# Kernel tuning notes

Measured on AMD Instinct MI355X. Metric: run time of the kernel, lower is better.

The kernel has to match this reference:

```python
import jax, jax.numpy as jnp
import numpy as np


def _lstm_layer(x, w_ih, w_hh, b_ih, b_hh):
    """Single PyTorch-style LSTM layer (gate order i,f,g,o). x: [B,T,D] -> [B,T,H]."""
    B, T, _ = x.shape
    H = w_hh.shape[1]
    # Precompute input projections for all timesteps (one big GEMM).
    xp = jnp.einsum('btd,gd->btg', x, w_ih) + b_ih + b_hh  # [B,T,4H]

    def step(carry, xt):
        h, c = carry
        gates = xt + h @ w_hh.T  # [B,4H]
        i, f, g, o = jnp.split(gates, 4, axis=-1)
        i = jax.nn.sigmoid(i)
        f = jax.nn.sigmoid(f)
        g = jnp.tanh(g)
        o = jax.nn.sigmoid(o)
        c = f * c + i * g
        h = o * jnp.tanh(c)
        return (h, c), h

    init = (jnp.zeros((B, H), x.dtype), jnp.zeros((B, H), x.dtype))
    _, hs = jax.lax.scan(step, init, jnp.swapaxes(xp, 0, 1))  # hs: [T,B,H]
    return jnp.swapaxes(hs, 0, 1)


def setup_inputs() -> dict:
    key = jax.random.key(0)
    ks = jax.random.split(key, 11)
    B, T, D, H, O = 256, 512, 64, 512, 1
    s_in = 1.0 / np.sqrt(H)
    inp = {
        'x': jax.random.normal(ks[0], (B, T, D), jnp.float32),
        'w_ih_0': jax.random.normal(ks[1], (4 * H, D), jnp.float32) * s_in,
        'w_hh_0': jax.random.normal(ks[2], (4 * H, H), jnp.float32) * s_in,
        'b_ih_0': jax.random.normal(ks[3], (4 * H,), jnp.float32) * s_in,
        'b_hh_0': jax.random.normal(ks[4], (4 * H,), jnp.float32) * s_in,
        'w_ih_1': jax.random.normal(ks[5], (4 * H, H), jnp.float32) * s_in,
        'w_hh_1': jax.random.normal(ks[6], (4 * H, H), jnp.float32) * s_in,
        'b_ih_1': jax.random.normal(ks[7], (4 * H,), jnp.float32) * s_in,
        'b_hh_1': jax.random.normal(ks[8], (4 * H,), jnp.float32) * s_in,
        'fc_w': jax.random.normal(ks[9], (O, H), jnp.float32) * s_in,
        'fc_b': jax.random.normal(ks[10], (O,), jnp.float32) * s_in,
    }
    return inp


def reference(x, w_ih_0, w_hh_0, b_ih_0, b_hh_0,
              w_ih_1, w_hh_1, b_ih_1, b_hh_1, fc_w, fc_b):
    h0 = _lstm_layer(x, w_ih_0, w_hh_0, b_ih_0, b_hh_0)   # [B,T,H]
    h1 = _lstm_layer(h0, w_ih_1, w_hh_1, b_ih_1, b_hh_1)  # [B,T,H]
    # fc on last timestep only
    return h1[:, -1, :] @ fc_w.T + fc_b  # [B,O]
```

## Files before the change

kernel.cpp:

```cpp
#include <hip/hip_runtime.h>


#define BATCH 256
#define SEQ   512
#define DIN   64
#define HID   512

typedef _Float16 f16_t;
typedef __attribute__((ext_vector_type(8))) _Float16 f16x8;
typedef __attribute__((ext_vector_type(4))) float    f32x4;

#define SCOPE_AGT __HIP_MEMORY_SCOPE_AGENT

__device__ inline f16x8 cvt8(const float* __restrict__ p) {
    f16x8 r;
#pragma unroll
    for (int j = 0; j < 8; j++) r[j] = (_Float16)p[j];
    return r;
}

__device__ inline f16x8 cvt8v(f32x4 lo, f32x4 hi) {
    f16x8 r;
#pragma unroll
    for (int j = 0; j < 4; j++) { r[j] = (_Float16)lo[j]; r[4 + j] = (_Float16)hi[j]; }
    return r;
}

__device__ inline f16x8 ldx8(const f16_t* p) {
    const unsigned long long* q = (const unsigned long long*)p;
    unsigned long long a = __hip_atomic_load(q,     __ATOMIC_RELAXED, SCOPE_AGT);
    unsigned long long b = __hip_atomic_load(q + 1, __ATOMIC_RELAXED, SCOPE_AGT);
    union { unsigned long long u[2]; f16x8 v; } c;
    c.u[0] = a; c.u[1] = b;
    return c.v;
}

__device__ inline void sth2a(f16_t* base_even, float h, float hn) {
    union { struct { _Float16 lo, hi; } s; unsigned u; } pk;
    pk.s.lo = (_Float16)h; pk.s.hi = (_Float16)hn;
    __hip_atomic_store((unsigned*)base_even, pk.u, __ATOMIC_RELAXED, SCOPE_AGT);
}

__device__ inline void pollw(const unsigned* p, unsigned need, int lane) {
    for (;;) {
        unsigned v = __hip_atomic_load(p + lane, __ATOMIC_RELAXED, SCOPE_AGT);
        if (__all((int)(v >= need))) break;
        __builtin_amdgcn_s_sleep(1);
    }
}

__device__ inline float sgm(float v) { return 1.f / (1.f + __expf(-v)); }
__device__ inline float th(float v)  { return 1.f - 2.f / (__expf(2.f * v) + 1.f); }

__global__ __launch_bounds__(256, 1) void lstm_pipe(
    const float* __restrict__ x,
    const float* __restrict__ wih0, const float* __restrict__ whh0,
    const float* __restrict__ bih0, const float* __restrict__ bhh0,
    const float* __restrict__ wih1, const float* __restrict__ whh1,
    const float* __restrict__ bih1, const float* __restrict__ bhh1,
    unsigned* __restrict__ f0m, unsigned* __restrict__ f1,
    f16_t* __restrict__ h1buf, f16_t* __restrict__ h0hist)
{
    __shared__ f32x4 red[5][17][64];

    const int tid  = threadIdx.x;
    const int w    = tid >> 6, lane = tid & 63;
    const int quad = lane >> 4, col = lane & 15;
    const int bid  = blockIdx.x;

    if (bid < 128) {
        const int g = bid & 7, s = bid >> 3;
        unsigned* myf = f0m + g * 64;
        const int mym = w & 1, myct = w >> 1;

        f16x8 Wh[32];
#pragma unroll
        for (int i = 0; i < 4; i++) {
            const int k0 = (w * 4 + i) * 32 + quad * 8;
#pragma unroll
            for (int ct = 0; ct < 2; ct++)
#pragma unroll
                for (int nt = 0; nt < 4; nt++) {
                    const int gr = nt * HID + s * 32 + ct * 16 + col;
                    Wh[i * 8 + ct * 4 + nt] = cvt8(whh0 + (size_t)gr * HID + k0);
                }
        }
        f16x8 Wx[8];
        if (w >= 2) {
#pragma unroll
            for (int ct = 0; ct < 2; ct++)
#pragma unroll
                for (int nt = 0; nt < 4; nt++) {
                    const int gr = nt * HID + s * 32 + ct * 16 + col;
                    Wx[ct * 4 + nt] = cvt8(wih0 + (size_t)gr * DIN + (w - 2) * 32 + quad * 8);
                }
        } else {
#pragma unroll
            for (int j = 0; j < 8; j++) Wx[j] = (f16x8)(_Float16)0;
        }
#pragma unroll
        for (int i = 0; i < 32; i++) asm volatile("" : "+v"(Wh[i]));
#pragma unroll
        for (int i = 0; i < 8; i++)  asm volatile("" : "+v"(Wx[i]));

        float bias[4];
#pragma unroll
        for (int nt = 0; nt < 4; nt++) {
            const int gr = nt * HID + s * 32 + myct * 16 + col;
            bias[nt] = bih0[gr] + bhh0[gr];
        }
        float cst[4] = {0, 0, 0, 0};

        for (int it = 0; it < SEQ; ++it) {
            {
                const f16_t* hw = h0hist + (size_t)it * BATCH * HID;
                unsigned sink = 0;
#pragma unroll
                for (int r = 0; r < 4; r++) {
                    const unsigned* p = (const unsigned*)(hw +
                        (size_t)(g * 32 + mym * 16 + quad * 4 + r) * HID + s * 32 + myct * 16 + (col & ~1));
                    sink += __hip_atomic_load(p, __ATOMIC_RELAXED, SCOPE_AGT);
                }
                asm volatile("" : "+v"(sink));
            }
            f32x4 xr[4];
            if (w >= 2) {
#pragma unroll
                for (int m = 0; m < 2; m++) {
                    const float* px = x + ((size_t)(g * 32 + m * 16 + col) * SEQ + it) * DIN + (w - 2) * 32 + quad * 8;
                    xr[m * 2]     = *(const f32x4*)px;
                    xr[m * 2 + 1] = *(const f32x4*)(px + 4);
                }
            }
            if (w == 0 && it >= 1) pollw(myf, (unsigned)it, lane);
            __syncthreads();

            f32x4 acc[16];
#pragma unroll
            for (int j = 0; j < 16; j++) acc[j] = (f32x4){0.f, 0.f, 0.f, 0.f};

            if (it > 0) {
                const f16_t* h0b = h0hist + (size_t)(it - 1) * BATCH * HID;
#pragma unroll
                for (int i = 0; i < 4; i++) {
                    const int kb = w * 4 + i;
#pragma unroll
                    for (int m = 0; m < 2; m++) {
                        f16x8 a = *(const f16x8*)(h0b + (size_t)(g * 32 + m * 16 + col) * HID + kb * 32 + quad * 8);
#pragma unroll
                        for (int ct = 0; ct < 2; ct++)
#pragma unroll
                            for (int nt = 0; nt < 4; nt++)
                                acc[m * 8 + ct * 4 + nt] = __builtin_amdgcn_mfma_f32_16x16x32_f16(
                                    a, Wh[i * 8 + ct * 4 + nt], acc[m * 8 + ct * 4 + nt], 0, 0, 0);
                    }
                }
            }
            if (w >= 2) {
#pragma unroll
                for (int m = 0; m < 2; m++) {
                    f16x8 a = cvt8v(xr[m * 2], xr[m * 2 + 1]);
#pragma unroll
                    for (int ct = 0; ct < 2; ct++)
#pragma unroll
                        for (int nt = 0; nt < 4; nt++)
                            acc[m * 8 + ct * 4 + nt] = __builtin_amdgcn_mfma_f32_16x16x32_f16(
                                a, Wx[ct * 4 + nt], acc[m * 8 + ct * 4 + nt], 0, 0, 0);
                }
            }
#pragma unroll
            for (int j = 0; j < 16; j++) red[w][j][lane] = acc[j];
            __syncthreads();

            f32x4 gate[4];
#pragma unroll
            for (int nt = 0; nt < 4; nt++) {
                f32x4 v = red[0][mym * 8 + myct * 4 + nt][lane];
#pragma unroll
                for (int ww = 1; ww < 4; ww++) {
                    f32x4 p = red[ww][mym * 8 + myct * 4 + nt][lane];
#pragma unroll
                    for (int r = 0; r < 4; r++) v[r] += p[r];
                }
                gate[nt] = v;
            }
            f16_t* hout = h0hist + (size_t)it * BATCH * HID;
#pragma unroll
            for (int r = 0; r < 4; r++) {
                float iv = sgm(gate[0][r] + bias[0]), fv = sgm(gate[1][r] + bias[1]);
                float gv = th(gate[2][r] + bias[2]),  ov = sgm(gate[3][r] + bias[3]);
                float c = fv * cst[r] + iv * gv;
                cst[r] = c;
                float h = ov * th(c);
                float hn = __shfl_down(h, 1);
                if ((lane & 1) == 0)
                    sth2a(hout + (size_t)(g * 32 + mym * 16 + quad * 4 + r) * HID + s * 32 + myct * 16 + col, h, hn);
            }
            asm volatile("s_waitcnt vmcnt(0)" ::: "memory");
            if (lane == 0)
                __hip_atomic_store(myf + s * 4 + mym * 2 + myct, (unsigned)(it + 1), __ATOMIC_RELAXED, SCOPE_AGT);
        }
    } else {
        const int idx = bid - 128;
        const int G = idx & 3, s1 = idx >> 2;
        unsigned* myf1 = f1 + G * 32;

        f16x8 Wb[32];
#pragma unroll
        for (int i = 0; i < 8; i++) {
            const int kb = w * 8 + i;
            const int k0 = kb * 32 + quad * 8;
#pragma unroll
            for (int nt = 0; nt < 4; nt++) {
                const int grow = nt * HID + s1 * 16 + col;
                const float* src = (kb < 16) ? (wih1 + (size_t)grow * HID + k0)
                                             : (whh1 + (size_t)grow * HID + (k0 - 512));
                Wb[i * 4 + nt] = cvt8(src);
            }
        }
#pragma unroll
        for (int i = 0; i < 32; i++) asm volatile("" : "+v"(Wb[i]));

        const int d = s1 * 16 + col;
        const float bi = bih1[d] + bhh1[d];
        const float bf = bih1[HID + d] + bhh1[HID + d];
        const float bg = bih1[2 * HID + d] + bhh1[2 * HID + d];
        const float bo = bih1[3 * HID + d] + bhh1[3 * HID + d];
        float cst[4] = {0, 0, 0, 0};

        for (int it = 1; it <= SEQ; ++it) {
            const int t = it - 1;
            if (w == 0) {
                const unsigned* pa = f0m + (2 * G) * 64;
                const unsigned* pb = f0m + (2 * G + 1) * 64;
                const bool chk = (it >= 2);
                for (;;) {
                    unsigned va = __hip_atomic_load(pa + lane, __ATOMIC_RELAXED, SCOPE_AGT);
                    unsigned vb = __hip_atomic_load(pb + lane, __ATOMIC_RELAXED, SCOPE_AGT);
                    unsigned vc = chk ? __hip_atomic_load(myf1 + (lane & 31), __ATOMIC_RELAXED, SCOPE_AGT)
                                      : 0xffffffffu;
                    if (__all((int)((va >= (unsigned)it) & (vb >= (unsigned)it) & (vc >= (unsigned)(it - 1))))) break;
                    __builtin_amdgcn_s_sleep(1);
                }
            }
            __syncthreads();

            f32x4 acc[16];
#pragma unroll
            for (int j = 0; j < 16; j++) acc[j] = (f32x4){0.f, 0.f, 0.f, 0.f};

            const f16_t* h0b = h0hist + (size_t)t * BATCH * HID;
            const f16_t* h1r = h1buf + (size_t)((t - 1) & 1) * BATCH * HID;
#pragma unroll
            for (int i = 0; i < 8; i++) {
                const int kb = w * 8 + i;
                if (kb < 16) {
#pragma unroll
                    for (int mt = 0; mt < 4; mt++) {
                        f16x8 a = *(const f16x8*)(h0b + (size_t)(G * 64 + mt * 16 + col) * HID + kb * 32 + quad * 8);
#pragma unroll
                        for (int nt = 0; nt < 4; nt++)
                            acc[mt * 4 + nt] = __builtin_amdgcn_mfma_f32_16x16x32_f16(
                                a, Wb[i * 4 + nt], acc[mt * 4 + nt], 0, 0, 0);
                    }
                } else if (t > 0) {
#pragma unroll
                    for (int mt = 0; mt < 4; mt++) {
                        f16x8 a = ldx8(h1r + (size_t)(G * 64 + mt * 16 + col) * HID + (kb - 16) * 32 + quad * 8);
#pragma unroll
                        for (int nt = 0; nt < 4; nt++)
                            acc[mt * 4 + nt] = __builtin_amdgcn_mfma_f32_16x16x32_f16(
                                a, Wb[i * 4 + nt], acc[mt * 4 + nt], 0, 0, 0);
                    }
                }
            }
#pragma unroll
            for (int j = 0; j < 16; j++) red[w][j][lane] = acc[j];
            __syncthreads();

            f32x4 gate[4];
#pragma unroll
            for (int nt = 0; nt < 4; nt++) {
                f32x4 v = red[0][w * 4 + nt][lane];
#pragma unroll
                for (int ww = 1; ww < 4; ww++) {
                    f32x4 p = red[ww][w * 4 + nt][lane];
#pragma unroll
                    for (int r = 0; r < 4; r++) v[r] += p[r];
                }
                gate[nt] = v;
            }
            f16_t* hout = h1buf + (size_t)(t & 1) * BATCH * HID;
#pragma unroll
            for (int r = 0; r < 4; r++) {
                float iv = sgm(gate[0][r] + bi), fv = sgm(gate[1][r] + bf);
                float gv = th(gate[2][r] + bg),  ov = sgm(gate[3][r] + bo);
                float c = fv * cst[r] + iv * gv;
                cst[r] = c;
                float h = ov * th(c);
                float hn = __shfl_down(h, 1);
                if ((lane & 1) == 0)
                    sth2a(hout + (size_t)(G * 64 + w * 16 + quad * 4 + r) * HID + s1 * 16 + col, h, hn);
            }
            __syncthreads();
            if (tid == 0)
                __hip_atomic_store(myf1 + s1, (unsigned)it, __ATOMIC_RELAXED, SCOPE_AGT);
        }
    }
}

__global__ void fc_k(const f16_t* __restrict__ h1buf, const float* __restrict__ fcw,
                     const float* __restrict__ fcb, float* __restrict__ out)
{
    const int b = blockIdx.x, lane = threadIdx.x;
    const f16_t* hp = h1buf + ((size_t)(BATCH + b)) * HID;
    float sum = 0.f;
#pragma unroll
    for (int j = 0; j < 8; j++) {
        const int k = lane * 8 + j;
        sum += (float)hp[k] * fcw[k];
    }
#pragma unroll
    for (int off = 32; off; off >>= 1) sum += __shfl_down(sum, off);
    if (lane == 0) out[b] = sum + fcb[0];
}

extern "C" void kernel_launch(void* const* d_in, const int* in_sizes, int n_in,
                              void* d_out, int out_size, void* d_ws, size_t ws_size,
                              hipStream_t stream)
{
    const float* x    = (const float*)d_in[0];
    const float* wih0 = (const float*)d_in[1];
    const float* whh0 = (const float*)d_in[2];
    const float* bih0 = (const float*)d_in[3];
    const float* bhh0 = (const float*)d_in[4];
    const float* wih1 = (const float*)d_in[5];
    const float* whh1 = (const float*)d_in[6];
    const float* bih1 = (const float*)d_in[7];
    const float* bhh1 = (const float*)d_in[8];
    const float* fcw  = (const float*)d_in[9];
    const float* fcb  = (const float*)d_in[10];
    float* out = (float*)d_out;

    unsigned char* ws = (unsigned char*)d_ws;
    unsigned* f0m = (unsigned*)ws;
    unsigned* f1  = (unsigned*)(ws + 2048);
    f16_t* h1buf  = (f16_t*)(ws + 4096);
    f16_t* h0hist = (f16_t*)(ws + 4096 + 2 * BATCH * HID * sizeof(f16_t));

    hipMemsetAsync(ws, 0, 4096, stream);
    lstm_pipe<<<dim3(256), dim3(256), 0, stream>>>(x, wih0, whh0, bih0, bhh0,
                                                   wih1, whh1, bih1, bhh1,
                                                   f0m, f1, h1buf, h0hist);
    fc_k<<<dim3(BATCH), dim3(64), 0, stream>>>(h1buf, fcw, fcb, out);
}
```

Measured before the change: 4.778 ms.

## Poll only needed producer flags per wave and drop a barrier via double-buffered reduction

Each wave now polls only the flags for the data it will read, so the step no longer waits on one poller wave followed by a block-wide barrier. The LDS reduction buffer is double-buffered by step parity so that removing the first __syncthreads does not let a fast wave overwrite partial sums still being read. In layer 1 the work is split into an h0 branch for waves 0-1 and an h1 branch for waves 2-3, each with its own wait condition. This shortens the per-step critical path across 512 sequential steps, but it puts more polling traffic on the flags and depends on the per-wave flag mapping being correct.

```diff
diff --git a/kernel.cpp b/kernel.cpp
--- a/kernel.cpp
+++ b/kernel.cpp
@@ -41,9 +41,9 @@
     __hip_atomic_store((unsigned*)base_even, pk.u, __ATOMIC_RELAXED, SCOPE_AGT);
 }
 
-__device__ inline void pollw(const unsigned* p, unsigned need, int lane) {
+__device__ inline void pollv(const unsigned* p, unsigned need) {
     for (;;) {
-        unsigned v = __hip_atomic_load(p + lane, __ATOMIC_RELAXED, SCOPE_AGT);
+        unsigned v = __hip_atomic_load(p, __ATOMIC_RELAXED, SCOPE_AGT);
         if (__all((int)(v >= need))) break;
         __builtin_amdgcn_s_sleep(1);
     }
@@ -61,7 +61,7 @@
     unsigned* __restrict__ f0m, unsigned* __restrict__ f1,
     f16_t* __restrict__ h1buf, f16_t* __restrict__ h0hist)
 {
-    __shared__ f32x4 red[5][17][64];
+    __shared__ f32x4 red[2][4][16][64];
 
     const int tid  = threadIdx.x;
     const int w    = tid >> 6, lane = tid & 63;
@@ -73,6 +73,9 @@
         unsigned* myf = f0m + g * 64;
         const int mym = w & 1, myct = w >> 1;
 
+        const int lp = lane & 15;
+        const unsigned* pollp = myf + (w * 4 + (lp >> 2)) * 4 + (lp & 3);
+
         f16x8 Wh[32];
 #pragma unroll
         for (int i = 0; i < 4; i++) {
@@ -132,8 +135,7 @@
                     xr[m * 2 + 1] = *(const f32x4*)(px + 4);
                 }
             }
-            if (w == 0 && it >= 1) pollw(myf, (unsigned)it, lane);
-            __syncthreads();
+            if (it >= 1) pollv(pollp, (unsigned)it);
 
             f32x4 acc[16];
 #pragma unroll
@@ -168,17 +170,18 @@
                                 a, Wx[ct * 4 + nt], acc[m * 8 + ct * 4 + nt], 0, 0, 0);
                 }
             }
-#pragma unroll
-            for (int j = 0; j < 16; j++) red[w][j][lane] = acc[j];
+            const int rb = it & 1;
+#pragma unroll
+            for (int j = 0; j < 16; j++) red[rb][w][j][lane] = acc[j];
             __syncthreads();
 
             f32x4 gate[4];
 #pragma unroll
             for (int nt = 0; nt < 4; nt++) {
-                f32x4 v = red[0][mym * 8 + myct * 4 + nt][lane];
+                f32x4 v = red[rb][0][mym * 8 + myct * 4 + nt][lane];
 #pragma unroll
                 for (int ww = 1; ww < 4; ww++) {
-                    f32x4 p = red[ww][mym * 8 + myct * 4 + nt][lane];
+                    f32x4 p = red[rb][ww][mym * 8 + myct * 4 + nt][lane];
 #pragma unroll
                     for (int r = 0; r < 4; r++) v[r] += p[r];
                 }
@@ -205,6 +208,10 @@
         const int G = idx & 3, s1 = idx >> 2;
         unsigned* myf1 = f1 + G * 32;
 
+        const unsigned* pollp = (w < 2)
+            ? (f0m + (size_t)(2 * G + (lane & 1)) * 64 + (w * 8 + (lane >> 3)) * 4 + ((lane >> 1) & 3))
+            : (myf1 + (lane & 31));
+
         f16x8 Wb[32];
 #pragma unroll
         for (int i = 0; i < 8; i++) {
@@ -230,20 +237,8 @@
 
         for (int it = 1; it <= SEQ; ++it) {
             const int t = it - 1;
-            if (w == 0) {
-                const unsigned* pa = f0m + (2 * G) * 64;
-                const unsigned* pb = f0m + (2 * G + 1) * 64;
-                const bool chk = (it >= 2);
-                for (;;) {
-                    unsigned va = __hip_atomic_load(pa + lane, __ATOMIC_RELAXED, SCOPE_AGT);
-                    unsigned vb = __hip_atomic_load(pb + lane, __ATOMIC_RELAXED, SCOPE_AGT);
-                    unsigned vc = chk ? __hip_atomic_load(myf1 + (lane & 31), __ATOMIC_RELAXED, SCOPE_AGT)
-                                      : 0xffffffffu;
-                    if (__all((int)((va >= (unsigned)it) & (vb >= (unsigned)it) & (vc >= (unsigned)(it - 1))))) break;
-                    __builtin_amdgcn_s_sleep(1);
-                }
-            }
-            __syncthreads();
+            if (w < 2) pollv(pollp, (unsigned)it);
+            else       pollv(pollp, (it >= 2) ? (unsigned)(it - 1) : 0u);
 
             f32x4 acc[16];
 #pragma unroll
@@ -251,10 +246,11 @@
 
             const f16_t* h0b = h0hist + (size_t)t * BATCH * HID;
             const f16_t* h1r = h1buf + (size_t)((t - 1) & 1) * BATCH * HID;
-#pragma unroll
-            for (int i = 0; i < 8; i++) {
-                const int kb = w * 8 + i;
-                if (kb < 16) {
+
+            if (w < 2) {
+#pragma unroll
+                for (int i = 0; i < 8; i++) {
+                    const int kb = w * 8 + i;
 #pragma unroll
                     for (int mt = 0; mt < 4; mt++) {
                         f16x8 a = *(const f16x8*)(h0b + (size_t)(G * 64 + mt * 16 + col) * HID + kb * 32 + quad * 8);
@@ -263,7 +259,11 @@
                             acc[mt * 4 + nt] = __builtin_amdgcn_mfma_f32_16x16x32_f16(
                                 a, Wb[i * 4 + nt], acc[mt * 4 + nt], 0, 0, 0);
                     }
-                } else if (t > 0) {
+                }
+            } else if (t > 0) {
+#pragma unroll
+                for (int i = 0; i < 8; i++) {
+                    const int kb = w * 8 + i;
 #pragma unroll
                     for (int mt = 0; mt < 4; mt++) {
                         f16x8 a = ldx8(h1r + (size_t)(G * 64 + mt * 16 + col) * HID + (kb - 16) * 32 + quad * 8);
@@ -274,17 +274,18 @@
                     }
                 }
             }
-#pragma unroll
-            for (int j = 0; j < 16; j++) red[w][j][lane] = acc[j];
+            const int rb = it & 1;
+#pragma unroll
+            for (int j = 0; j < 16; j++) red[rb][w][j][lane] = acc[j];
             __syncthreads();
 
             f32x4 gate[4];
 #pragma unroll
             for (int nt = 0; nt < 4; nt++) {
-                f32x4 v = red[0][w * 4 + nt][lane];
+                f32x4 v = red[rb][0][w * 4 + nt][lane];
 #pragma unroll
                 for (int ww = 1; ww < 4; ww++) {
-                    f32x4 p = red[ww][w * 4 + nt][lane];
+                    f32x4 p = red[rb][ww][w * 4 + nt][lane];
 #pragma unroll
                     for (int r = 0; r < 4; r++) v[r] += p[r];
                 }
```

Measured after the change: 5.577 ms. +16.7%, slower.

## Replace full layer-0 history with 8-slot ring buffer and batch A-operand loads

Applied to the files above, without the earlier changes.

Layer-0 hidden states go into an 8-slot ring instead of a full SEQ-length history, so the working set stays cache-resident. Layer-0 blocks now also poll layer-1 progress flags as backpressure so a slot is not overwritten before it is consumed. The prefetch-touch of the next history slot is removed, and the A-operand loads in both layers are hoisted into register arrays (atomic relaxed loads) ahead of the MFMA loops to overlap memory latency. The extra cross-layer wait can stall layer 0 when layer 1 lags, and the larger register arrays add register pressure.

```diff
diff --git a/kernel.cpp b/kernel.cpp
--- a/kernel.cpp
+++ b/kernel.cpp
@@ -41,14 +41,6 @@
     __hip_atomic_store((unsigned*)base_even, pk.u, __ATOMIC_RELAXED, SCOPE_AGT);
 }
 
-__device__ inline void pollw(const unsigned* p, unsigned need, int lane) {
-    for (;;) {
-        unsigned v = __hip_atomic_load(p + lane, __ATOMIC_RELAXED, SCOPE_AGT);
-        if (__all((int)(v >= need))) break;
-        __builtin_amdgcn_s_sleep(1);
-    }
-}
-
 __device__ inline float sgm(float v) { return 1.f / (1.f + __expf(-v)); }
 __device__ inline float th(float v)  { return 1.f - 2.f / (__expf(2.f * v) + 1.f); }
 
@@ -59,7 +51,7 @@
     const float* __restrict__ wih1, const float* __restrict__ whh1,
     const float* __restrict__ bih1, const float* __restrict__ bhh1,
     unsigned* __restrict__ f0m, unsigned* __restrict__ f1,
-    f16_t* __restrict__ h1buf, f16_t* __restrict__ h0hist)
+    f16_t* __restrict__ h1buf, f16_t* __restrict__ h0ring)
 {
     __shared__ f32x4 red[5][17][64];
 
@@ -72,6 +64,7 @@
         const int g = bid & 7, s = bid >> 3;
         unsigned* myf = f0m + g * 64;
         const int mym = w & 1, myct = w >> 1;
+        const unsigned* bp = f1 + (size_t)(g >> 1) * 32 + (lane & 31);
 
         f16x8 Wh[32];
 #pragma unroll
@@ -112,17 +105,6 @@
         float cst[4] = {0, 0, 0, 0};
 
         for (int it = 0; it < SEQ; ++it) {
-            {
-                const f16_t* hw = h0hist + (size_t)it * BATCH * HID;
-                unsigned sink = 0;
-#pragma unroll
-                for (int r = 0; r < 4; r++) {
-                    const unsigned* p = (const unsigned*)(hw +
-                        (size_t)(g * 32 + mym * 16 + quad * 4 + r) * HID + s * 32 + myct * 16 + (col & ~1));
-                    sink += __hip_atomic_load(p, __ATOMIC_RELAXED, SCOPE_AGT);
-                }
-                asm volatile("" : "+v"(sink));
-            }
             f32x4 xr[4];
             if (w >= 2) {
 #pragma unroll
@@ -132,7 +114,15 @@
                     xr[m * 2 + 1] = *(const f32x4*)(px + 4);
                 }
             }
-            if (w == 0 && it >= 1) pollw(myf, (unsigned)it, lane);
+            if (w == 0 && it >= 1) {
+                const unsigned nb = (it >= 8) ? (unsigned)(it - 7) : 0u;
+                for (;;) {
+                    unsigned v  = __hip_atomic_load(myf + lane, __ATOMIC_RELAXED, SCOPE_AGT);
+                    unsigned b2 = __hip_atomic_load(bp,         __ATOMIC_RELAXED, SCOPE_AGT);
+                    if (__all((int)((v >= (unsigned)it) & (b2 >= nb)))) break;
+                    __builtin_amdgcn_s_sleep(1);
+                }
+            }
             __syncthreads();
 
             f32x4 acc[16];
@@ -140,21 +130,24 @@
             for (int j = 0; j < 16; j++) acc[j] = (f32x4){0.f, 0.f, 0.f, 0.f};
 
             if (it > 0) {
-                const f16_t* h0b = h0hist + (size_t)(it - 1) * BATCH * HID;
-#pragma unroll
-                for (int i = 0; i < 4; i++) {
-                    const int kb = w * 4 + i;
-#pragma unroll
-                    for (int m = 0; m < 2; m++) {
-                        f16x8 a = *(const f16x8*)(h0b + (size_t)(g * 32 + m * 16 + col) * HID + kb * 32 + quad * 8);
+                const f16_t* h0b = h0ring + (size_t)((it - 1) & 7) * BATCH * HID;
+                f16x8 ab[8];
+#pragma unroll
+                for (int i = 0; i < 4; i++)
+#pragma unroll
+                    for (int m = 0; m < 2; m++)
+                        ab[i * 2 + m] = ldx8(h0b + (size_t)(g * 32 + m * 16 + col) * HID
+                                             + (w * 4 + i) * 32 + quad * 8);
+#pragma unroll
+                for (int i = 0; i < 4; i++)
+#pragma unroll
+                    for (int m = 0; m < 2; m++)
 #pragma unroll
                         for (int ct = 0; ct < 2; ct++)
 #pragma unroll
                             for (int nt = 0; nt < 4; nt++)
                                 acc[m * 8 + ct * 4 + nt] = __builtin_amdgcn_mfma_f32_16x16x32_f16(
-                                    a, Wh[i * 8 + ct * 4 + nt], acc[m * 8 + ct * 4 + nt], 0, 0, 0);
-                    }
-                }
+                                    ab[i * 2 + m], Wh[i * 8 + ct * 4 + nt], acc[m * 8 + ct * 4 + nt], 0, 0, 0);
             }
             if (w >= 2) {
 #pragma unroll
@@ -184,7 +177,7 @@
                 }
                 gate[nt] = v;
             }
-            f16_t* hout = h0hist + (size_t)it * BATCH * HID;
+            f16_t* hout = h0ring + (size_t)(it & 7) * BATCH * HID;
 #pragma unroll
             for (int r = 0; r < 4; r++) {
                 float iv = sgm(gate[0][r] + bias[0]), fv = sgm(gate[1][r] + bias[1]);
@@ -249,30 +242,41 @@
 #pragma unroll
             for (int j = 0; j < 16; j++) acc[j] = (f32x4){0.f, 0.f, 0.f, 0.f};
 
-            const f16_t* h0b = h0hist + (size_t)t * BATCH * HID;
+            const f16_t* h0b = h0ring + (size_t)(t & 7) * BATCH * HID;
             const f16_t* h1r = h1buf + (size_t)((t - 1) & 1) * BATCH * HID;
-#pragma unroll
-            for (int i = 0; i < 8; i++) {
-                const int kb = w * 8 + i;
-                if (kb < 16) {
-#pragma unroll
-                    for (int mt = 0; mt < 4; mt++) {
-                        f16x8 a = *(const f16x8*)(h0b + (size_t)(G * 64 + mt * 16 + col) * HID + kb * 32 + quad * 8);
+
+            if (w < 2) {
+                f16x8 ab[32];
+#pragma unroll
+                for (int i = 0; i < 8; i++)
+#pragma unroll
+                    for (int mt = 0; mt < 4; mt++)
+                        ab[i * 4 + mt] = ldx8(h0b + (size_t)(G * 64 + mt * 16 + col) * HID
+                                              + (w * 8 + i) * 32 + quad * 8);
+#pragma unroll
+                for (int i = 0; i < 8; i++)
+#pragma unroll
+                    for (int mt = 0; mt < 4; mt++)
 #pragma unroll
                         for (int nt = 0; nt < 4; nt++)
                             acc[mt * 4 + nt] = __builtin_amdgcn_mfma_f32_16x16x32_f16(
-                                a, Wb[i * 4 + nt], acc[mt * 4 + nt], 0, 0, 0);
-                    }
-                } else if (t > 0) {
-#pragma unroll
-                    for (int mt = 0; mt < 4; mt++) {
-                        f16x8 a = ldx8(h1r + (size_t)(G * 64 + mt * 16 + col) * HID + (kb - 16) * 32 + quad * 8);
+                                ab[i * 4 + mt], Wb[i * 4 + nt], acc[mt * 4 + nt], 0, 0, 0);
+            } else if (t > 0) {
+                f16x8 ab[32];
+#pragma unroll
+                for (int i = 0; i < 8; i++)
+#pragma unroll
+                    for (int mt = 0; mt < 4; mt++)
+                        ab[i * 4 + mt] = ldx8(h1r + (size_t)(G * 64 + mt * 16 + col) * HID
+                                              + (w * 8 + i - 16) * 32 + quad * 8);
+#pragma unroll
+                for (int i = 0; i < 8; i++)
+#pragma unroll
+                    for (int mt = 0; mt < 4; mt++)
 #pragma unroll
                         for (int nt = 0; nt < 4; nt++)
                             acc[mt * 4 + nt] = __builtin_amdgcn_mfma_f32_16x16x32_f16(
-                                a, Wb[i * 4 + nt], acc[mt * 4 + nt], 0, 0, 0);
-                    }
-                }
+                                ab[i * 4 + mt], Wb[i * 4 + nt], acc[mt * 4 + nt], 0, 0, 0);
             }
 #pragma unroll
             for (int j = 0; j < 16; j++) red[w][j][lane] = acc[j];
@@ -346,11 +350,11 @@
     unsigned* f0m = (unsigned*)ws;
     unsigned* f1  = (unsigned*)(ws + 2048);
     f16_t* h1buf  = (f16_t*)(ws + 4096);
-    f16_t* h0hist = (f16_t*)(ws + 4096 + 2 * BATCH * HID * sizeof(f16_t));
+    f16_t* h0ring = (f16_t*)(ws + 4096 + 2 * BATCH * HID * sizeof(f16_t));
 
     hipMemsetAsync(ws, 0, 4096, stream);
     lstm_pipe<<<dim3(256), dim3(256), 0, stream>>>(x, wih0, whh0, bih0, bhh0,
                                                    wih1, whh1, bih1, bhh1,
-                                                   f0m, f1, h1buf, h0hist);
+                                                   f0m, f1, h1buf, h0ring);
     fc_k<<<dim3(BATCH), dim3(64), 0, stream>>>(h1buf, fcw, fcb, out);
 }
```

Result: slower. 5.601 ms (+17.2%).
